# Kernel optimization log

Measured on AMD Instinct MI355X. Metric: run time of the kernel, lower is better.

## Reference

```python
import jax, jax.numpy as jnp
import numpy as np


def setup_inputs() -> dict:
    key = jax.random.key(0)
    k1, k2, k3, k4 = jax.random.split(key, 4)
    B, M, N = 8, 4096, 4096
    return {
        "pc_src": jax.random.normal(k1, (B, 3, M), dtype=jnp.float32),
        "pc_dst": jax.random.normal(k2, (B, 3, N), dtype=jnp.float32),
        "sigma_src": jax.random.uniform(k3, (B, M), dtype=jnp.float32),
        "sigma_dst": jax.random.uniform(k4, (B, N), dtype=jnp.float32),
    }


def reference(pc_src, pc_dst, sigma_src, sigma_dst):
    # Pairwise Euclidean distance: diff[b, m, n] = ||pc_src[b,:,m] - pc_dst[b,:,n]||_2
    d = pc_src[:, :, :, None] - pc_dst[:, :, None, :]  # [B, 3, M, N]
    diff = jnp.sqrt(jnp.sum(d * d, axis=1))            # [B, M, N]

    # src -> dst
    src_dst_min_dist = jnp.min(diff, axis=2)           # [B, M]
    src_dst_I = jnp.argmin(diff, axis=2)               # [B, M]
    selected_sigma_dst = jnp.take_along_axis(sigma_dst, src_dst_I, axis=1)
    sigma_src_dst = (sigma_src + selected_sigma_dst) / 2
    forward_loss = jnp.mean(src_dst_min_dist * sigma_src_dst)

    # dst -> src
    dst_src_min_dist = jnp.min(diff, axis=1)           # [B, N]
    dst_src_I = jnp.argmin(diff, axis=1)               # [B, N]
    selected_sigma_src = jnp.take_along_axis(sigma_src, dst_src_I, axis=1)
    sigma_dst_src = (sigma_dst + selected_sigma_src) / 2
    backward_loss = jnp.mean(dst_src_min_dist * sigma_dst_src)

    return forward_loss + backward_loss
```

## Files before the change

kernel.cpp:

```cpp
#include <hip/hip_runtime.h>
#include <math.h>
#include <cfloat>

#define BLOCK 256
#define QPT 8

__global__ __launch_bounds__(BLOCK, 4)
void chamfer_min_kernel(const float* __restrict__ pc_src,
                        const float* __restrict__ pc_dst,
                        unsigned* __restrict__ part0,
                        unsigned* __restrict__ part1,
                        int M, int N, int B, int RC,
                        float* out_zero) {
    extern __shared__ float4 lds[];
    const int b = blockIdx.y;
    const int zc = blockIdx.z;
    const int dir = (zc >= RC) ? 1 : 0;
    const int chunk = zc - dir * RC;

    const int NQ = dir ? N : M;
    const int NR = dir ? M : N;
    const float* pcq = dir ? pc_dst : pc_src;
    const float* pcr = dir ? pc_src : pc_dst;
    unsigned* part = dir ? part1 : part0;

    const int CS = NR / RC;
    const int n0 = chunk * CS;
    const int tid = threadIdx.x;

    if (out_zero && blockIdx.x == 0 && b == 0 && zc == 0 && tid == 0)
        *out_zero = 0.0f;

    const float* rbase = pcr + (size_t)b * 3 * NR;
    for (int i = tid; i < CS; i += BLOCK) {
        const float rx = rbase[n0 + i];
        const float ry = rbase[NR + n0 + i];
        const float rz = rbase[2 * NR + n0 + i];
        lds[i] = make_float4(-2.0f * rx, -2.0f * ry, -2.0f * rz,
                             fmaf(rx, rx, fmaf(ry, ry, rz * rz)) + 64.0f);
    }

    const int q0 = blockIdx.x * (BLOCK * QPT) + tid;
    const float* qbase = pcq + (size_t)b * 3 * NQ;
    float qx[QPT], qy[QPT], qz[QPT];
    unsigned kmin[QPT];
#pragma unroll
    for (int j = 0; j < QPT; ++j) {
        const int q = q0 + j * BLOCK;
        qx[j] = qbase[q];
        qy[j] = qbase[NQ + q];
        qz[j] = qbase[2 * NQ + q];
        kmin[j] = 0xFFFFFFFFu;
    }

    __syncthreads();

    const unsigned mask = ~(unsigned)(CS - 1);
#pragma unroll 4
    for (int i = 0; i < CS; ++i) {
        const float4 r = lds[i];
#pragma unroll
        for (int j = 0; j < QPT; ++j) {
            float e = fmaf(qx[j], r.x, r.w);
            e = fmaf(qy[j], r.y, e);
            e = fmaf(qz[j], r.z, e);
            const unsigned key = (__float_as_uint(e) & mask) | (unsigned)i;
            kmin[j] = (key < kmin[j]) ? key : kmin[j];
        }
    }

#pragma unroll
    for (int j = 0; j < QPT; ++j) {
        const int q = q0 + j * BLOCK;
        part[((size_t)chunk * B + b) * NQ + q] = kmin[j];
    }
}

__global__ void chamfer_reduce_kernel(const float* __restrict__ pc_src,
                                      const float* __restrict__ pc_dst,
                                      const float* __restrict__ sig_src,
                                      const float* __restrict__ sig_dst,
                                      const unsigned* __restrict__ part0,
                                      const unsigned* __restrict__ part1,
                                      float* __restrict__ out,
                                      int M, int N, int B, int RC) {
    __shared__ float red[BLOCK];
    const int TT = blockIdx.x * BLOCK + threadIdx.x;
    const int dir = (TT >= B * M);
    const int t = dir ? TT - B * M : TT;

    const int NQ = dir ? N : M;
    const int NR = dir ? M : N;
    const float* pcq  = dir ? pc_dst : pc_src;
    const float* pcr  = dir ? pc_src : pc_dst;
    const float* sigq = dir ? sig_dst : sig_src;
    const float* sigr = dir ? sig_src : sig_dst;
    const unsigned* part = dir ? part1 : part0;
    const float scale = 1.0f / (float)(B * NQ);
    const int CS = NR / RC;

    const int b = t / NQ;
    const int q = t - b * NQ;

    unsigned kbest = 0xFFFFFFFFu;
    int cbest = 0;
    for (int c = 0; c < RC; ++c) {
        const unsigned k = part[((size_t)c * B + b) * NQ + q];
        if (k < kbest) { kbest = k; cbest = c; }
    }
    const int gidx = cbest * CS + (int)(kbest & (unsigned)(CS - 1));

    const float* qbase = pcq + (size_t)b * 3 * NQ;
    const float* rbase = pcr + (size_t)b * 3 * NR;
    const float dx = qbase[q]          - rbase[gidx];
    const float dy = qbase[NQ + q]     - rbase[NR + gidx];
    const float dz = qbase[2 * NQ + q] - rbase[2 * NR + gidx];
    const float dist = sqrtf(fmaf(dx, dx, fmaf(dy, dy, dz * dz)));

    const float s = 0.5f * (sigq[t] + sigr[(size_t)b * NR + gidx]);
    red[threadIdx.x] = dist * s * scale;
    __syncthreads();

    for (int w = BLOCK / 2; w > 0; w >>= 1) {
        if (threadIdx.x < w) red[threadIdx.x] += red[threadIdx.x + w];
        __syncthreads();
    }
    if (threadIdx.x == 0) atomicAdd(out, red[0]);
}

extern "C" void kernel_launch(void* const* d_in, const int* in_sizes, int n_in,
                              void* d_out, int out_size, void* d_ws, size_t ws_size,
                              hipStream_t stream) {
    const float* pc_src  = (const float*)d_in[0];
    const float* pc_dst  = (const float*)d_in[1];
    const float* sig_src = (const float*)d_in[2];
    const float* sig_dst = (const float*)d_in[3];
    float* out = (float*)d_out;

    const int B = 8;
    const int M = in_sizes[2] / B;
    const int N = in_sizes[3] / B;
    const int NMAX = (M > N) ? M : N;

    int RC = 64;
    while (RC > 1 && 2 * (size_t)B * NMAX * RC * sizeof(unsigned) > ws_size) RC >>= 1;

    unsigned* part0 = (unsigned*)d_ws;
    unsigned* part1 = part0 + (size_t)RC * B * NMAX;

    {
        const int CSMAX = NMAX / RC;
        dim3 grid(NMAX / (BLOCK * QPT), B, 2 * RC);
        chamfer_min_kernel<<<grid, BLOCK, CSMAX * sizeof(float4), stream>>>(
            pc_src, pc_dst, part0, part1, M, N, B, RC, out);
    }
    {
        dim3 rgrid((B * (M + N)) / BLOCK);
        chamfer_reduce_kernel<<<rgrid, BLOCK, 0, stream>>>(
            pc_src, pc_dst, sig_src, sig_dst, part0, part1, out, M, N, B, RC);
    }
}
```

Baseline: 61.90 us.

## Use packed FMA, fixed 64-point chunks, and 64-bit atomicMin merge of partial minima

Switches the inner distance loop to v_pk_fma_f32 so two reference points are evaluated per instruction. Reference chunks become a fixed 64 points, giving many more blocks, and per-chunk partial minima are merged in the min kernel with a 64-bit atomicMin instead of being written to partial buffers and scanned in the reduce kernel. Adds two memsets and heavy atomic traffic, and truncating the distance key to 26 bits (6 index bits in the low end) may change which point wins ties.

```diff
diff --git a/kernel.cpp b/kernel.cpp
--- a/kernel.cpp
+++ b/kernel.cpp
@@ -4,52 +4,66 @@
 
 #define BLOCK 256
 #define QPT 8
+#define CS  64
+
+typedef float f32x2 __attribute__((ext_vector_type(2)));
+typedef float f32x4 __attribute__((ext_vector_type(4)));
+typedef unsigned long long u64;
+
+static __device__ __forceinline__ unsigned umin32(unsigned a, unsigned b) {
+    return a < b ? a : b;
+}
+static __device__ __forceinline__ f32x2 vlo(f32x4 v) { return __builtin_shufflevector(v, v, 0, 1); }
+static __device__ __forceinline__ f32x2 vhi(f32x4 v) { return __builtin_shufflevector(v, v, 2, 3); }
 
 __global__ __launch_bounds__(BLOCK, 4)
 void chamfer_min_kernel(const float* __restrict__ pc_src,
                         const float* __restrict__ pc_dst,
-                        unsigned* __restrict__ part0,
-                        unsigned* __restrict__ part1,
-                        int M, int N, int B, int RC,
-                        float* out_zero) {
-    extern __shared__ float4 lds[];
+                        u64* __restrict__ part,
+                        int M, int N, int B, int Zn) {
+    __shared__ f32x4 lds4[CS];
+
     const int b = blockIdx.y;
-    const int zc = blockIdx.z;
-    const int dir = (zc >= RC) ? 1 : 0;
-    const int chunk = zc - dir * RC;
+    const int z = blockIdx.z;
+    const int dir = (z >= Zn) ? 1 : 0;
+    const int chunk = dir ? (z - Zn) : z;
 
     const int NQ = dir ? N : M;
     const int NR = dir ? M : N;
     const float* pcq = dir ? pc_dst : pc_src;
     const float* pcr = dir ? pc_src : pc_dst;
-    unsigned* part = dir ? part1 : part0;
+    u64* pp = part + (dir ? (size_t)B * M : (size_t)0) + (size_t)b * NQ;
 
-    const int CS = NR / RC;
     const int n0 = chunk * CS;
     const int tid = threadIdx.x;
 
-    if (out_zero && blockIdx.x == 0 && b == 0 && zc == 0 && tid == 0)
-        *out_zero = 0.0f;
-
-    const float* rbase = pcr + (size_t)b * 3 * NR;
-    for (int i = tid; i < CS; i += BLOCK) {
-        const float rx = rbase[n0 + i];
-        const float ry = rbase[NR + n0 + i];
-        const float rz = rbase[2 * NR + n0 + i];
-        lds[i] = make_float4(-2.0f * rx, -2.0f * ry, -2.0f * rz,
-                             fmaf(rx, rx, fmaf(ry, ry, rz * rz)) + 64.0f);
+    const float* rbase = pcr + (size_t)b * 3 * NR + n0;
+    if (tid < CS / 2) {
+        const int p = tid;
+        const f32x2 rx = *(const f32x2*)(rbase + 2 * p);
+        const f32x2 ry = *(const f32x2*)(rbase + NR + 2 * p);
+        const f32x2 rz = *(const f32x2*)(rbase + 2 * NR + 2 * p);
+        f32x4 w0, w1;
+        w0.x = -2.0f * rx.x; w0.y = -2.0f * rx.y;
+        w0.z = -2.0f * ry.x; w0.w = -2.0f * ry.y;
+        w1.x = -2.0f * rz.x; w1.y = -2.0f * rz.y;
+        w1.z = fmaf(rx.x, rx.x, fmaf(ry.x, ry.x, rz.x * rz.x)) + 64.0f;
+        w1.w = fmaf(rx.y, rx.y, fmaf(ry.y, ry.y, rz.y * rz.y)) + 64.0f;
+        lds4[2 * p]     = w0;
+        lds4[2 * p + 1] = w1;
     }
 
     const int q0 = blockIdx.x * (BLOCK * QPT) + tid;
-    const float* qbase = pcq + (size_t)b * 3 * NQ;
-    float qx[QPT], qy[QPT], qz[QPT];
+    const float* qb = pcq + (size_t)b * 3 * NQ;
+    f32x2 qx2[QPT], qy2[QPT], qz2[QPT];
     unsigned kmin[QPT];
 #pragma unroll
     for (int j = 0; j < QPT; ++j) {
         const int q = q0 + j * BLOCK;
-        qx[j] = qbase[q];
-        qy[j] = qbase[NQ + q];
-        qz[j] = qbase[2 * NQ + q];
+        const float x = qb[q], y = qb[NQ + q], zz = qb[2 * NQ + q];
+        qx2[j] = (f32x2){x, x};
+        qy2[j] = (f32x2){y, y};
+        qz2[j] = (f32x2){zz, zz};
         kmin[j] = 0xFFFFFFFFu;
     }
 
@@ -57,22 +71,32 @@
 
     const unsigned mask = ~(unsigned)(CS - 1);
 #pragma unroll 4
-    for (int i = 0; i < CS; ++i) {
-        const float4 r = lds[i];
+    for (int p = 0; p < CS / 2; ++p) {
+        const f32x4 w0 = lds4[2 * p];
+        const f32x4 w1 = lds4[2 * p + 1];
+        const f32x2 rx2 = vlo(w0), ry2 = vhi(w0);
+        const f32x2 rz2 = vlo(w1), rw2 = vhi(w1);
 #pragma unroll
         for (int j = 0; j < QPT; ++j) {
-            float e = fmaf(qx[j], r.x, r.w);
-            e = fmaf(qy[j], r.y, e);
-            e = fmaf(qz[j], r.z, e);
-            const unsigned key = (__float_as_uint(e) & mask) | (unsigned)i;
-            kmin[j] = (key < kmin[j]) ? key : kmin[j];
+            f32x2 e;
+            asm("v_pk_fma_f32 %0, %1, %2, %3"
+                : "=v"(e) : "v"(qz2[j]), "v"(rz2), "v"(rw2));
+            asm("v_pk_fma_f32 %0, %1, %2, %0"
+                : "+v"(e) : "v"(qy2[j]), "v"(ry2));
+            asm("v_pk_fma_f32 %0, %1, %2, %0"
+                : "+v"(e) : "v"(qx2[j]), "v"(rx2));
+            const unsigned k0 = (__float_as_uint(e.x) & mask) | (unsigned)(2 * p);
+            const unsigned k1 = (__float_as_uint(e.y) & mask) | (unsigned)(2 * p + 1);
+            kmin[j] = umin32(umin32(k0, k1), kmin[j]);
         }
     }
 
 #pragma unroll
     for (int j = 0; j < QPT; ++j) {
         const int q = q0 + j * BLOCK;
-        part[((size_t)chunk * B + b) * NQ + q] = kmin[j];
+        const unsigned gidx = (unsigned)n0 + (kmin[j] & (unsigned)(CS - 1));
+        const u64 key = ((u64)(kmin[j] & mask) << 32) | (u64)gidx;
+        atomicMin(&pp[q], key);
     }
 }
 
@@ -80,10 +104,9 @@
                                       const float* __restrict__ pc_dst,
                                       const float* __restrict__ sig_src,
                                       const float* __restrict__ sig_dst,
-                                      const unsigned* __restrict__ part0,
-                                      const unsigned* __restrict__ part1,
+                                      const u64* __restrict__ part,
                                       float* __restrict__ out,
-                                      int M, int N, int B, int RC) {
+                                      int M, int N, int B) {
     __shared__ float red[BLOCK];
     const int TT = blockIdx.x * BLOCK + threadIdx.x;
     const int dir = (TT >= B * M);
@@ -95,20 +118,12 @@
     const float* pcr  = dir ? pc_src : pc_dst;
     const float* sigq = dir ? sig_dst : sig_src;
     const float* sigr = dir ? sig_src : sig_dst;
-    const unsigned* part = dir ? part1 : part0;
     const float scale = 1.0f / (float)(B * NQ);
-    const int CS = NR / RC;
 
     const int b = t / NQ;
     const int q = t - b * NQ;
 
-    unsigned kbest = 0xFFFFFFFFu;
-    int cbest = 0;
-    for (int c = 0; c < RC; ++c) {
-        const unsigned k = part[((size_t)c * B + b) * NQ + q];
-        if (k < kbest) { kbest = k; cbest = c; }
-    }
-    const int gidx = cbest * CS + (int)(kbest & (unsigned)(CS - 1));
+    const int gidx = (int)(unsigned)part[TT];
 
     const float* qbase = pcq + (size_t)b * 3 * NQ;
     const float* rbase = pcr + (size_t)b * 3 * NR;
@@ -142,21 +157,23 @@
     const int N = in_sizes[3] / B;
     const int NMAX = (M > N) ? M : N;
 
-    int RC = 64;
-    while (RC > 1 && 2 * (size_t)B * NMAX * RC * sizeof(unsigned) > ws_size) RC >>= 1;
+    const int Zn = N / CS;
+    const int Zm = M / CS;
 
-    unsigned* part0 = (unsigned*)d_ws;
-    unsigned* part1 = part0 + (size_t)RC * B * NMAX;
+    u64* part = (u64*)d_ws;
+    const size_t partBytes = (size_t)B * (M + N) * sizeof(u64);
+
+    hipMemsetAsync(part, 0xFF, partBytes, stream);
+    hipMemsetAsync(d_out, 0, sizeof(float), stream);
 
     {
-        const int CSMAX = NMAX / RC;
-        dim3 grid(NMAX / (BLOCK * QPT), B, 2 * RC);
-        chamfer_min_kernel<<<grid, BLOCK, CSMAX * sizeof(float4), stream>>>(
-            pc_src, pc_dst, part0, part1, M, N, B, RC, out);
+        dim3 grid(NMAX / (BLOCK * QPT), B, Zn + Zm);
+        chamfer_min_kernel<<<grid, BLOCK, 0, stream>>>(
+            pc_src, pc_dst, part, M, N, B, Zn);
     }
     {
         dim3 rgrid((B * (M + N)) / BLOCK);
         chamfer_reduce_kernel<<<rgrid, BLOCK, 0, stream>>>(
-            pc_src, pc_dst, sig_src, sig_dst, part0, part1, out, M, N, B, RC);
+            pc_src, pc_dst, sig_src, sig_dst, part, out, M, N, B);
     }
 }
```

Measured after the change: 49.89 us. 19.4% less time.
